# Performance work log

Hardware: AMD Instinct MI355X
Metric: run time of the kernel (lower is better)

## Reference

```python
import jax, jax.numpy as jnp
import numpy as np

# Product fuzzy logic (embed-wise):
#   bin_xnor(a,b)    = a*b + (1-a)*(1-b)
#   implies(a,b)     = 1 - a*(1-b)
#   conjoin(x,dim)   = prod(x, dim)
#   bin_conjoin(a,b) = a*b
#   disjoin(x,dim)   = 1 - prod(1-x, dim)

B, IN_F, HID_F, OUT_F, E = 128, 256, 512, 128, 8

def setup_inputs() -> dict:
    key = jax.random.key(0)
    k0, k1, k2, k3 = jax.random.split(key, 4)
    return {
        "input": jax.random.uniform(k0, (B, IN_F, E), dtype=jnp.float32),
        "conj_weights": jax.random.uniform(k1, (IN_F, HID_F, E), dtype=jnp.float32),
        "conj_signs": jax.random.uniform(k2, (IN_F, HID_F, E), dtype=jnp.float32),
        "disj_weights": jax.random.uniform(k3, (HID_F, OUT_F, E), dtype=jnp.float32),
    }

def reference(input, conj_weights, conj_signs, disj_weights):
    # --- EmbedSignedConjunction ---
    x = input[:, :, None, :]                      # [B, in, 1, E]
    xnor = x * conj_signs + (1.0 - x) * (1.0 - conj_signs)   # [B, in, hid, E]
    impl = 1.0 - conj_weights * (1.0 - xnor)      # implies(w, xnor)
    h = jnp.prod(impl, axis=1)                    # conjoin over in -> [B, hid, E]

    # --- EmbedUnsignedDisjunction ---
    hh = h[:, :, None, :]                         # [B, hid, 1, E]
    conj = disj_weights * hh                      # bin_conjoin -> [B, hid, out, E]
    out = 1.0 - jnp.prod(1.0 - conj, axis=1)      # disjoin over hid -> [B, out, E]
    return out
```

## Files before the change

### kernel.cpp

```cpp
#include <hip/hip_runtime.h>


__global__ __launch_bounds__(128, 2) void k_stage1(
    const float* __restrict__ in,
    const float* __restrict__ cw,
    const float* __restrict__ cs,
    float* __restrict__ Hout)
{
    __shared__ float lds[8192];
    const int t  = threadIdx.x;
    const int hl = t & 7;
    const int ck = t >> 3;
    const int hg = blockIdx.x & 63;
    const int bp = blockIdx.x >> 6;
    const int h  = hg * 8 + hl;
    const int b0 = bp * 8;

    float acc[8][8];
    #pragma unroll
    for (int b = 0; b < 8; ++b)
        #pragma unroll
        for (int e = 0; e < 8; ++e) acc[b][e] = 1.0f;

    const float* pw = cw + (ck * 16) * 4096 + h * 8;
    const float* ps = cs + (ck * 16) * 4096 + h * 8;
    const float* px = in + b0 * 2048 + (ck * 16) * 8;

    #pragma unroll 2
    for (int ii = 0; ii < 16; ++ii) {
        float wv[8], sv[8], Av[8], Bv[8];
        *(float4*)(wv)     = *(const float4*)(pw);
        *(float4*)(wv + 4) = *(const float4*)(pw + 4);
        *(float4*)(sv)     = *(const float4*)(ps);
        *(float4*)(sv + 4) = *(const float4*)(ps + 4);
        pw += 4096; ps += 4096;
        #pragma unroll
        for (int e = 0; e < 8; ++e) {
            const float p = wv[e] * sv[e];
            Av[e] = 1.0f - p;
            Bv[e] = fmaf(2.0f, p, -wv[e]);
        }
        #pragma unroll
        for (int b = 0; b < 8; ++b) {
            float xv[8];
            *(float4*)(xv)     = *(const float4*)(px + b * 2048);
            *(float4*)(xv + 4) = *(const float4*)(px + b * 2048 + 4);
            #pragma unroll
            for (int e = 0; e < 8; ++e)
                acc[b][e] *= fmaf(xv[e], Bv[e], Av[e]);
        }
        px += 8;
    }

    #pragma unroll
    for (int b = 0; b < 8; ++b)
        #pragma unroll
        for (int e = 0; e < 8; ++e)
            lds[((hl * 64 + b * 8 + e) << 4) + ck] = acc[b][e];
    __syncthreads();

    const int oid = t * 4;
    const int hlo = oid >> 6, bo = (oid >> 3) & 7, e0 = oid & 7;
    float4 r;
    float* pr = &r.x;
    #pragma unroll
    for (int j = 0; j < 4; ++j) {
        const float* q = &lds[((hlo * 64 + bo * 8 + e0 + j) << 4)];
        float m = 1.0f;
        #pragma unroll
        for (int c = 0; c < 16; ++c) m *= q[c];
        pr[j] = m;
    }
    *(float4*)(Hout + (b0 + bo) * 4096 + (hg * 8 + hlo) * 8 + e0) = r;
}

__global__ __launch_bounds__(512, 4) void k_stage2(
    const float* __restrict__ dw,
    const float* __restrict__ H,
    float* __restrict__ out)
{
    __shared__ float lds[8736];
    const int t  = threadIdx.x;
    const int ol = t & 31;
    const int hc = t >> 5;
    const int og = blockIdx.x & 3;
    const int bg = blockIdx.x >> 2;
    const int o  = og * 32 + ol;
    const int b0 = bg * 2;

    float acc[2][8];
    #pragma unroll
    for (int bb = 0; bb < 2; ++bb)
        #pragma unroll
        for (int e = 0; e < 8; ++e) acc[bb][e] = 1.0f;

    const float* pd = dw + (hc * 32) * 1024 + o * 8;
    const float* ph = H + b0 * 4096 + (hc * 32) * 8;

    #pragma unroll 2
    for (int ii = 0; ii < 32; ++ii) {
        float dv[8];
        *(float4*)(dv)     = *(const float4*)(pd);
        *(float4*)(dv + 4) = *(const float4*)(pd + 4);
        pd += 1024;
        #pragma unroll
        for (int bb = 0; bb < 2; ++bb) {
            float hv[8];
            *(float4*)(hv)     = *(const float4*)(ph + bb * 4096);
            *(float4*)(hv + 4) = *(const float4*)(ph + bb * 4096 + 4);
            #pragma unroll
            for (int e = 0; e < 8; ++e)
                acc[bb][e] *= fmaf(-dv[e], hv[e], 1.0f);
        }
        ph += 8;
    }

    #pragma unroll
    for (int bb = 0; bb < 2; ++bb)
        #pragma unroll
        for (int e = 0; e < 8; ++e)
            lds[ol * 273 + (bb * 8 + e) * 17 + hc] = acc[bb][e];
    __syncthreads();

    const int eo = t & 7, bo = (t >> 3) & 1, olo = t >> 4;
    const float* q = &lds[olo * 273 + (bo * 8 + eo) * 17];
    float m = 1.0f;
    #pragma unroll
    for (int c = 0; c < 16; ++c) m *= q[c];
    out[(b0 + bo) * 1024 + (og * 32 + olo) * 8 + eo] = 1.0f - m;
}

extern "C" void kernel_launch(void* const* d_in, const int* in_sizes, int n_in,
                              void* d_out, int out_size, void* d_ws, size_t ws_size,
                              hipStream_t stream)
{
    const float* in = (const float*)d_in[0];
    const float* cw = (const float*)d_in[1];
    const float* cs = (const float*)d_in[2];
    const float* dw = (const float*)d_in[3];
    float* out = (float*)d_out;
    float* H   = (float*)d_ws;

    k_stage1<<<1024, 128, 0, stream>>>(in, cw, cs, H);
    k_stage2<<<256, 512, 0, stream>>>(dw, H, out);
}
```

Before: 110.4 us.

## Retile both stages with float2 packed math and finer thread decomposition

Stage 1 now gives each thread 2 hidden units by 2 embed lanes over 8 batches, uses 256-thread blocks, and writes partial products to LDS in a padded layout so the reduction reads coalesced float2 values. Stage 2 is retiled so each thread computes 4 outputs by 4 batches on 2 embed lanes, splitting the hidden dimension 32 ways with 512 blocks of 256 threads. The float2 helpers are meant to let the compiler emit packed FP32 multiply and FMA and cut per-thread register pressure for higher occupancy. The cost is narrower float2 global loads in place of float4 and more partial products to reduce through LDS.

```diff
diff --git a/kernel.cpp b/kernel.cpp
--- a/kernel.cpp
+++ b/kernel.cpp
@@ -1,133 +1,149 @@
 #include <hip/hip_runtime.h>
 
 
-__global__ __launch_bounds__(128, 2) void k_stage1(
+static inline __device__ float2 f2mul(float2 a, float2 b) {
+    return make_float2(a.x * b.x, a.y * b.y);
+}
+static inline __device__ float2 f2fma(float2 a, float2 b, float2 c) {
+    return make_float2(fmaf(a.x, b.x, c.x), fmaf(a.y, b.y, c.y));
+}
+static inline __device__ float2 f2nfma1(float2 d, float2 h) {
+    return make_float2(fmaf(-d.x, h.x, 1.0f), fmaf(-d.y, h.y, 1.0f));
+}
+
+__global__ __launch_bounds__(256, 4) void k_stage1(
     const float* __restrict__ in,
     const float* __restrict__ cw,
     const float* __restrict__ cs,
     float* __restrict__ Hout)
 {
-    __shared__ float lds[8192];
+    __shared__ float lds[16 * 520];
     const int t  = threadIdx.x;
-    const int hl = t & 7;
-    const int ck = t >> 3;
-    const int hg = blockIdx.x & 63;
-    const int bp = blockIdx.x >> 6;
-    const int h  = hg * 8 + hl;
+    const int hl = t & 3;
+    const int eg = (t >> 2) & 3;
+    const int ck = t >> 4;
+    const int bp = blockIdx.x & 15;
+    const int hg = blockIdx.x >> 4;
     const int b0 = bp * 8;
+    const int h0 = hg * 8 + hl * 2;
+    const int e0 = eg * 2;
+    const int i0 = ck * 16;
 
-    float acc[8][8];
+    float2 acc[8][2];
     #pragma unroll
-    for (int b = 0; b < 8; ++b)
-        #pragma unroll
-        for (int e = 0; e < 8; ++e) acc[b][e] = 1.0f;
+    for (int b = 0; b < 8; ++b) {
+        acc[b][0] = make_float2(1.0f, 1.0f);
+        acc[b][1] = make_float2(1.0f, 1.0f);
+    }
 
-    const float* pw = cw + (ck * 16) * 4096 + h * 8;
-    const float* ps = cs + (ck * 16) * 4096 + h * 8;
-    const float* px = in + b0 * 2048 + (ck * 16) * 8;
+    const float* pw = cw + i0 * 4096 + h0 * 8 + e0;
+    const float* ps = cs + i0 * 4096 + h0 * 8 + e0;
+    const float* px = in + b0 * 2048 + i0 * 8 + e0;
 
-    #pragma unroll 2
+    #pragma unroll 4
     for (int ii = 0; ii < 16; ++ii) {
-        float wv[8], sv[8], Av[8], Bv[8];
-        *(float4*)(wv)     = *(const float4*)(pw);
-        *(float4*)(wv + 4) = *(const float4*)(pw + 4);
-        *(float4*)(sv)     = *(const float4*)(ps);
-        *(float4*)(sv + 4) = *(const float4*)(ps + 4);
+        const float2 w0 = *(const float2*)(pw);
+        const float2 w1 = *(const float2*)(pw + 8);
+        const float2 s0 = *(const float2*)(ps);
+        const float2 s1 = *(const float2*)(ps + 8);
         pw += 4096; ps += 4096;
-        #pragma unroll
-        for (int e = 0; e < 8; ++e) {
-            const float p = wv[e] * sv[e];
-            Av[e] = 1.0f - p;
-            Bv[e] = fmaf(2.0f, p, -wv[e]);
-        }
+        const float2 p0 = f2mul(w0, s0);
+        const float2 p1 = f2mul(w1, s1);
+        const float2 A0 = make_float2(1.0f - p0.x, 1.0f - p0.y);
+        const float2 A1 = make_float2(1.0f - p1.x, 1.0f - p1.y);
+        const float2 B0 = make_float2(p0.x + p0.x - w0.x, p0.y + p0.y - w0.y);
+        const float2 B1 = make_float2(p1.x + p1.x - w1.x, p1.y + p1.y - w1.y);
         #pragma unroll
         for (int b = 0; b < 8; ++b) {
-            float xv[8];
-            *(float4*)(xv)     = *(const float4*)(px + b * 2048);
-            *(float4*)(xv + 4) = *(const float4*)(px + b * 2048 + 4);
-            #pragma unroll
-            for (int e = 0; e < 8; ++e)
-                acc[b][e] *= fmaf(xv[e], Bv[e], Av[e]);
+            const float2 xv = *(const float2*)(px + b * 2048);
+            acc[b][0] = f2mul(acc[b][0], f2fma(xv, B0, A0));
+            acc[b][1] = f2mul(acc[b][1], f2fma(xv, B1, A1));
         }
         px += 8;
     }
 
     #pragma unroll
-    for (int b = 0; b < 8; ++b)
+    for (int b = 0; b < 8; ++b) {
         #pragma unroll
-        for (int e = 0; e < 8; ++e)
-            lds[((hl * 64 + b * 8 + e) << 4) + ck] = acc[b][e];
+        for (int hh = 0; hh < 2; ++hh) {
+            const int out = b * 64 + (hl * 2 + hh) * 8 + e0;
+            *(float2*)&lds[ck * 520 + out] = acc[b][hh];
+        }
+    }
     __syncthreads();
 
-    const int oid = t * 4;
-    const int hlo = oid >> 6, bo = (oid >> 3) & 7, e0 = oid & 7;
-    float4 r;
-    float* pr = &r.x;
-    #pragma unroll
-    for (int j = 0; j < 4; ++j) {
-        const float* q = &lds[((hlo * 64 + bo * 8 + e0 + j) << 4)];
-        float m = 1.0f;
+    {
+        const int o2 = t * 2;
+        float2 m = *(const float2*)&lds[o2];
         #pragma unroll
-        for (int c = 0; c < 16; ++c) m *= q[c];
-        pr[j] = m;
+        for (int c = 1; c < 16; ++c)
+            m = f2mul(m, *(const float2*)&lds[c * 520 + o2]);
+        const int b = o2 >> 6;
+        const int rem = o2 & 63;
+        *(float2*)(Hout + (b0 + b) * 4096 + hg * 64 + rem) = m;
     }
-    *(float4*)(Hout + (b0 + bo) * 4096 + (hg * 8 + hlo) * 8 + e0) = r;
 }
 
-__global__ __launch_bounds__(512, 4) void k_stage2(
+__global__ __launch_bounds__(256, 4) void k_stage2(
     const float* __restrict__ dw,
-    const float* __restrict__ H,
+    const float* __restrict__ Hin,
     float* __restrict__ out)
 {
-    __shared__ float lds[8736];
+    __shared__ float lds[32 * 264];
     const int t  = threadIdx.x;
-    const int ol = t & 31;
-    const int hc = t >> 5;
-    const int og = blockIdx.x & 3;
-    const int bg = blockIdx.x >> 2;
-    const int o  = og * 32 + ol;
-    const int b0 = bg * 2;
+    const int ol = t & 1;
+    const int eg = (t >> 1) & 3;
+    const int hc = t >> 3;
+    const int bg = blockIdx.x & 31;
+    const int og = blockIdx.x >> 5;
+    const int b0 = bg * 4;
+    const int o0 = og * 8 + ol * 4;
+    const int e0 = eg * 2;
+    const int h0 = hc * 16;
 
-    float acc[2][8];
+    float2 acc[4][4];
     #pragma unroll
-    for (int bb = 0; bb < 2; ++bb)
+    for (int oo = 0; oo < 4; ++oo)
         #pragma unroll
-        for (int e = 0; e < 8; ++e) acc[bb][e] = 1.0f;
+        for (int bb = 0; bb < 4; ++bb)
+            acc[oo][bb] = make_float2(1.0f, 1.0f);
 
-    const float* pd = dw + (hc * 32) * 1024 + o * 8;
-    const float* ph = H + b0 * 4096 + (hc * 32) * 8;
+    const float* pd = dw + h0 * 1024 + o0 * 8 + e0;
+    const float* ph = Hin + b0 * 4096 + h0 * 8 + e0;
 
-    #pragma unroll 2
-    for (int ii = 0; ii < 32; ++ii) {
-        float dv[8];
-        *(float4*)(dv)     = *(const float4*)(pd);
-        *(float4*)(dv + 4) = *(const float4*)(pd + 4);
-        pd += 1024;
+    #pragma unroll 4
+    for (int ii = 0; ii < 16; ++ii) {
+        float2 dv[4], hv[4];
         #pragma unroll
-        for (int bb = 0; bb < 2; ++bb) {
-            float hv[8];
-            *(float4*)(hv)     = *(const float4*)(ph + bb * 4096);
-            *(float4*)(hv + 4) = *(const float4*)(ph + bb * 4096 + 4);
+        for (int oo = 0; oo < 4; ++oo) dv[oo] = *(const float2*)(pd + oo * 8);
+        #pragma unroll
+        for (int bb = 0; bb < 4; ++bb) hv[bb] = *(const float2*)(ph + bb * 4096);
+        pd += 1024; ph += 8;
+        #pragma unroll
+        for (int oo = 0; oo < 4; ++oo)
             #pragma unroll
-            for (int e = 0; e < 8; ++e)
-                acc[bb][e] *= fmaf(-dv[e], hv[e], 1.0f);
-        }
-        ph += 8;
+            for (int bb = 0; bb < 4; ++bb)
+                acc[oo][bb] = f2mul(acc[oo][bb], f2nfma1(dv[oo], hv[bb]));
     }
 
     #pragma unroll
-    for (int bb = 0; bb < 2; ++bb)
+    for (int oo = 0; oo < 4; ++oo) {
         #pragma unroll
-        for (int e = 0; e < 8; ++e)
-            lds[ol * 273 + (bb * 8 + e) * 17 + hc] = acc[bb][e];
+        for (int bb = 0; bb < 4; ++bb) {
+            const int o_l = ol * 4 + oo;
+            const int idx = bb * 64 + o_l * 8 + e0;
+            *(float2*)&lds[hc * 264 + idx] = acc[oo][bb];
+        }
+    }
     __syncthreads();
 
-    const int eo = t & 7, bo = (t >> 3) & 1, olo = t >> 4;
-    const float* q = &lds[olo * 273 + (bo * 8 + eo) * 17];
-    float m = 1.0f;
-    #pragma unroll
-    for (int c = 0; c < 16; ++c) m *= q[c];
-    out[(b0 + bo) * 1024 + (og * 32 + olo) * 8 + eo] = 1.0f - m;
+    {
+        float m = lds[t];
+        #pragma unroll
+        for (int c = 1; c < 32; ++c)
+            m *= lds[c * 264 + t];
+        out[(b0 + (t >> 6)) * 1024 + og * 64 + (t & 63)] = 1.0f - m;
+    }
 }
 
 extern "C" void kernel_launch(void* const* d_in, const int* in_sizes, int n_in,
@@ -138,9 +154,9 @@
     const float* cw = (const float*)d_in[1];
     const float* cs = (const float*)d_in[2];
     const float* dw = (const float*)d_in[3];
-    float* out = (float*)d_out;
-    float* H   = (float*)d_ws;
+    float* outp = (float*)d_out;
+    float* H    = (float*)d_ws;
 
-    k_stage1<<<1024, 128, 0, stream>>>(in, cw, cs, H);
-    k_stage2<<<256, 512, 0, stream>>>(dw, H, out);
+    k_stage1<<<1024, 256, 0, stream>>>(in, cw, cs, H);
+    k_stage2<<<512, 256, 0, stream>>>(dw, H, outp);
 }
```

Result: slower. 116.1 us (+5.1%).
